# Kernel tuning notes

Hardware: AMD Instinct MI355X
Metric: run time of the kernel (lower is better)

Reference implementation:

```python
import jax, jax.numpy as jnp
import numpy as np

N_NODES = 50000
N_EDGES = 800000
K_HOPS = 4
F_IN, F_HID, A_DIM = 6, 128, 3


def gcn_norm(edge_index, edge_weight, num_nodes):
    # TAGConv(normalize=True) uses gcn_norm WITHOUT added self-loops:
    # norm = D^{-1/2}[src] * w * D^{-1/2}[dst], deg computed at target (col).
    row, col = edge_index[0], edge_index[1]
    deg = jax.ops.segment_sum(edge_weight, col, num_segments=num_nodes)
    deg_inv_sqrt = jnp.where(deg > 0, jax.lax.rsqrt(deg), 0.0)
    return deg_inv_sqrt[row] * edge_weight * deg_inv_sqrt[col]


def tag_conv(x, edge_index, norm_w, W, b):
    # out = sum_{k=0..K} (A_hat^k x) @ W[k] + b ; W: [K+1, in, out]
    row, col = edge_index[0], edge_index[1]
    out = x @ W[0]
    xk = x
    for k in range(1, W.shape[0]):
        # one sparse propagation hop: gather at src, scale, scatter-add at dst
        xk = jax.ops.segment_sum(norm_w[:, None] * xk[row], col, num_segments=x.shape[0])
        out = out + xk @ W[k]
    return out + b


def setup_inputs() -> dict:
    key = jax.random.key(0)
    ks = jax.random.split(key, 5)
    x = jax.random.normal(ks[0], (N_NODES, F_IN), dtype=jnp.float32)
    edge_index = jax.random.randint(ks[1], (2, N_EDGES), 0, N_NODES, dtype=jnp.int32)
    edge_weight = jax.random.uniform(ks[2], (N_EDGES,), dtype=jnp.float32)
    s1 = float(1.0 / np.sqrt(F_IN))
    s2 = float(1.0 / np.sqrt(F_HID))
    W1 = jax.random.uniform(ks[3], (K_HOPS + 1, F_IN, F_HID), minval=-s1, maxval=s1, dtype=jnp.float32)
    b1 = jnp.zeros((F_HID,), jnp.float32)
    W2 = jax.random.uniform(ks[4], (K_HOPS + 1, F_HID, 2 * A_DIM), minval=-s2, maxval=s2, dtype=jnp.float32)
    b2 = jnp.zeros((2 * A_DIM,), jnp.float32)
    return {"x": x, "edge_index": edge_index, "edge_weight": edge_weight,
            "W1": W1, "b1": b1, "W2": W2, "b2": b2}


def reference(x, edge_index, edge_weight, W1, b1, W2, b2):
    norm_w = gcn_norm(edge_index, edge_weight, x.shape[0])
    h = jax.nn.relu(tag_conv(x, edge_index, norm_w, W1, b1))
    out = tag_conv(h, edge_index, norm_w, W2, b2)
    mu = jnp.tanh(out[..., :A_DIM])
    logvar = jnp.tanh(out[..., A_DIM:])
    sigma = jnp.exp(2.0 * logvar)
    return mu, sigma
```

## Files before the change

kernel.cpp:

```cpp
#include <hip/hip_runtime.h>

#define NN 50000
#define NE 800000
#define KH 4
#define FIN 6
#define FH 128
#define FO 6
#define ADIM 3
#define NN6 (NN * 6)
#define NN8 (NN * 8)
#define NBKT 196
#define EPB 2048
#define NPB 391
#define CAP 6144
#define ROWMASK 0xFFFFFu
#define GFUSE 2048
#define NEPAD (NE + NBKT * 1024)

typedef unsigned int u32;
typedef _Float16 f16;
typedef f16 f16x8 __attribute__((ext_vector_type(8)));

struct __align__(8) Edge { u32 r; float w; };

__device__ __forceinline__ float h2f_bits(u32 hb) {
    union { unsigned short us; f16 h; } c; c.us = (unsigned short)hb; return (float)c.h;
}
__device__ __forceinline__ u32 f2h_bits(float f) {
    union { unsigned short us; f16 h; } c; c.h = (f16)f; return (u32)c.us;
}
__device__ __forceinline__ u32 pack2(float a, float b) {
    return f2h_bits(a) | (f2h_bits(b) << 16);
}

__global__ void bucket_hist(const int* __restrict__ col, u32* __restrict__ ghist) {
    __shared__ u32 h[NBKT];
    for (int t = threadIdx.x; t < NBKT; t += 256) h[t] = 0;
    __syncthreads();
    int base = blockIdx.x * EPB;
#pragma unroll
    for (int i = 0; i < EPB / 256; ++i) {
        int e = base + i * 256 + threadIdx.x;
        if (e < NE) atomicAdd(&h[((u32)col[e]) >> 8], 1u);
    }
    __syncthreads();
    for (int t = threadIdx.x; t < NBKT; t += 256)
        if (h[t]) atomicAdd(&ghist[t], h[t]);
}

__global__ void bucket_scan(const u32* __restrict__ ghist, u32* __restrict__ bbase,
                            u32* __restrict__ bcur) {
    __shared__ u32 sh[256];
    int t = threadIdx.x;
    u32 v = (t < NBKT) ? ghist[t] : 0;
    sh[t] = v;
    __syncthreads();
    for (int off = 1; off < 256; off <<= 1) {
        u32 u = (t >= off) ? sh[t - off] : 0;
        __syncthreads();
        sh[t] += u;
        __syncthreads();
    }
    if (t < NBKT) { bbase[t] = sh[t] - v; bcur[t] = sh[t] - v; }
    if (t == NBKT - 1) bbase[NBKT] = sh[t];
}

__global__ __launch_bounds__(256) void partition_kernel(
        const int* __restrict__ row, const int* __restrict__ col,
        const float* __restrict__ w, u32* __restrict__ bcur,
        Edge* __restrict__ etmp) {
    __shared__ u32 hcnt[NBKT];
    __shared__ u32 hloc[NBKT];
    __shared__ u32 hglb[NBKT];
    __shared__ u32 smeta[EPB];
    __shared__ float swt[EPB];
    __shared__ u32 sgid[EPB];
    __shared__ u32 sc[256];
    for (int t = threadIdx.x; t < NBKT; t += 256) hcnt[t] = 0;
    __syncthreads();
    int base = blockIdx.x * EPB;
    u32 m_[8]; float w_[8]; u32 b_[8]; u32 rk_[8]; int v_[8];
#pragma unroll
    for (int i = 0; i < 8; ++i) {
        int e = base + i * 256 + threadIdx.x;
        v_[i] = e < NE;
        if (v_[i]) {
            u32 c = (u32)col[e];
            u32 r = (u32)row[e];
            b_[i] = c >> 8;
            m_[i] = ((c & 255u) << 20) | r;
            w_[i] = w[e];
            rk_[i] = atomicAdd(&hcnt[b_[i]], 1u);
        }
    }
    __syncthreads();
    {
        int t = threadIdx.x;
        u32 v = (t < NBKT) ? hcnt[t] : 0;
        sc[t] = v;
        __syncthreads();
        for (int off = 1; off < 256; off <<= 1) {
            u32 u = (t >= off) ? sc[t - off] : 0;
            __syncthreads();
            sc[t] += u;
            __syncthreads();
        }
        if (t < NBKT) hloc[t] = sc[t] - v;
    }
    __syncthreads();
    for (int t = threadIdx.x; t < NBKT; t += 256)
        if (hcnt[t]) hglb[t] = atomicAdd(&bcur[t], hcnt[t]);
    __syncthreads();
#pragma unroll
    for (int i = 0; i < 8; ++i) if (v_[i]) {
        u32 slot = hloc[b_[i]] + rk_[i];
        smeta[slot] = m_[i];
        swt[slot] = w_[i];
        sgid[slot] = hglb[b_[i]] + rk_[i];
    }
    __syncthreads();
    int tot = NE - base; if (tot > EPB) tot = EPB;
    for (int s = threadIdx.x; s < tot; s += 256) {
        Edge ed; ed.r = smeta[s]; ed.w = swt[s];
        etmp[sgid[s]] = ed;
    }
}

__global__ __launch_bounds__(256) void bucket_csr(
        const u32* __restrict__ bbase, const Edge* __restrict__ etmp,
        u32* __restrict__ edges, int* __restrict__ offs, int* __restrict__ eoff,
        float* __restrict__ dinv) {
    int b = blockIdx.x;
    int t = threadIdx.x;
    u32 s = bbase[b], e = bbase[b + 1];
    int cnt = (int)(e - s);
    u32 rb = s + (u32)b * 1024u;
    int node0 = b << 8;
    int nloc = NN - node0; if (nloc > 256) nloc = 256;
    __shared__ u32 ncnt[256];
    __shared__ float nsum[256];
    __shared__ u32 ncur[256];
    __shared__ u32 sc[256];
    __shared__ u32 stage[CAP];
    ncnt[t] = 0; nsum[t] = 0.f;
    __syncthreads();
    for (int i = t; i < cnt; i += 256) {
        Edge ed = etmp[s + i];
        u32 cl = ed.r >> 20;
        atomicAdd(&ncnt[cl], 1u);
        atomicAdd(&nsum[cl], ed.w);
    }
    __syncthreads();
    u32 v = ncnt[t];
    u32 pv = (v + 3u) & ~3u;
    sc[t] = pv;
    __syncthreads();
    for (int off = 1; off < 256; off <<= 1) {
        u32 u = (t >= off) ? sc[t - off] : 0;
        __syncthreads();
        sc[t] += u;
        __syncthreads();
    }
    u32 excl = sc[t] - pv;
    u32 ptot = sc[255];
    ncur[t] = excl;
    if (t < nloc) {
        offs[node0 + t] = (int)(rb + excl);
        eoff[node0 + t] = (int)(rb + excl + pv);
        float d = nsum[t];
        dinv[node0 + t] = d > 0.f ? rsqrtf(d) : 0.f;
    }
    __syncthreads();
    for (int i = t; i < cnt; i += 256) {
        Edge ed = etmp[s + i];
        u32 cl = ed.r >> 20;
        u32 slot = atomicAdd(&ncur[cl], 1u);
        u32 pw = (ed.r & ROWMASK) | (f2h_bits(ed.w) << 16);
        if (slot < CAP) stage[slot] = pw;
        else edges[rb + slot] = pw;
    }
    if (t < nloc) {
        for (u32 slot = excl + v; slot < excl + pv; ++slot) {
            if (slot < CAP) stage[slot] = 0u;
            else edges[rb + slot] = 0u;
        }
    }
    __syncthreads();
    int lim = (int)(ptot < CAP ? ptot : CAP);
    for (int i = t; i < lim; i += 256) edges[rb + i] = stage[i];
}

__global__ void pad_x(const float* __restrict__ x, f16* __restrict__ xpad) {
    int t = blockIdx.x * blockDim.x + threadIdx.x;
    if (t >= NN8) return;
    int n = t >> 3, c = t & 7;
    xpad[t] = (c < 6) ? (f16)x[n * 6 + c] : (f16)0.f;
}

__device__ __forceinline__ void gath(const f16* __restrict__ xp, u32 r, float w,
                                     float& a0, float& a1, float& a2,
                                     float& a3, float& a4, float& a5) {
    f16x8 v = *(const f16x8*)(xp + (size_t)r * 8);
    a0 += w * (float)v[0]; a1 += w * (float)v[1]; a2 += w * (float)v[2];
    a3 += w * (float)v[3]; a4 += w * (float)v[4]; a5 += w * (float)v[5];
}

#define HOP_HEAD \
    int t = blockIdx.x * blockDim.x + threadIdx.x; \
    int n = t >> 2, j = t & 3; \
    if (n >= NN) return; \
    int s = offs[n], e = eoff[n]; \
    float a0 = 0.f, a1 = 0.f, a2 = 0.f, a3 = 0.f, a4 = 0.f, a5 = 0.f;

#define HOP_REDUCE \
    _Pragma("unroll") \
    for (int d = 1; d < 4; d <<= 1) { \
        a0 += __shfl_xor(a0, d); a1 += __shfl_xor(a1, d); a2 += __shfl_xor(a2, d); \
        a3 += __shfl_xor(a3, d); a4 += __shfl_xor(a4, d); a5 += __shfl_xor(a5, d); \
    }

__global__ void hop4(const int* __restrict__ offs, const int* __restrict__ eoff,
                     const u32* __restrict__ edges,
                     const f16* __restrict__ xprev, const float* __restrict__ yadd,
                     f16* __restrict__ xnext) {
    HOP_HEAD
    for (int i = s + 4 * j; i < e; i += 16) {
        int4 q = *(const int4*)(edges + i);
        { u32 wd = (u32)q.x; gath(xprev, wd & 0xFFFFu, h2f_bits(wd >> 16), a0, a1, a2, a3, a4, a5); }
        { u32 wd = (u32)q.y; gath(xprev, wd & 0xFFFFu, h2f_bits(wd >> 16), a0, a1, a2, a3, a4, a5); }
        { u32 wd = (u32)q.z; gath(xprev, wd & 0xFFFFu, h2f_bits(wd >> 16), a0, a1, a2, a3, a4, a5); }
        { u32 wd = (u32)q.w; gath(xprev, wd & 0xFFFFu, h2f_bits(wd >> 16), a0, a1, a2, a3, a4, a5); }
    }
    HOP_REDUCE
    float v0 = j == 0 ? a0 : j == 1 ? a2 : j == 2 ? a4 : 0.f;
    float v1 = j == 0 ? a1 : j == 1 ? a3 : j == 2 ? a5 : 0.f;
    if (yadd && j < 3) {
        v0 += yadd[(size_t)n * 32 + 2 * j];
        v1 += yadd[(size_t)n * 32 + 2 * j + 1];
    }
    ((u32*)xnext)[(size_t)n * 4 + j] = pack2(v0, v1);
}

__global__ void hop4_norm(const int* __restrict__ offs, const int* __restrict__ eoff,
                          u32* __restrict__ edges,
                          const float* __restrict__ dinv, const f16* __restrict__ xpad,
                          f16* __restrict__ xnext) {
    HOP_HEAD
    float dn = dinv[n];
    for (int i = s + 4 * j; i < e; i += 16) {
        int4 q = *(const int4*)(edges + i);
        int4 nq;
        {
            u32 wd = (u32)q.x; u32 r = wd & 0xFFFFu;
            float wn = h2f_bits(wd >> 16) * dn * dinv[r];
            nq.x = (int)(r | (f2h_bits(wn) << 16));
            gath(xpad, r, wn, a0, a1, a2, a3, a4, a5);
        }
        {
            u32 wd = (u32)q.y; u32 r = wd & 0xFFFFu;
            float wn = h2f_bits(wd >> 16) * dn * dinv[r];
            nq.y = (int)(r | (f2h_bits(wn) << 16));
            gath(xpad, r, wn, a0, a1, a2, a3, a4, a5);
        }
        {
            u32 wd = (u32)q.z; u32 r = wd & 0xFFFFu;
            float wn = h2f_bits(wd >> 16) * dn * dinv[r];
            nq.z = (int)(r | (f2h_bits(wn) << 16));
            gath(xpad, r, wn, a0, a1, a2, a3, a4, a5);
        }
        {
            u32 wd = (u32)q.w; u32 r = wd & 0xFFFFu;
            float wn = h2f_bits(wd >> 16) * dn * dinv[r];
            nq.w = (int)(r | (f2h_bits(wn) << 16));
            gath(xpad, r, wn, a0, a1, a2, a3, a4, a5);
        }
        *(int4*)(edges + i) = nq;
    }
    HOP_REDUCE
    float v0 = j == 0 ? a0 : j == 1 ? a2 : j == 2 ? a4 : 0.f;
    float v1 = j == 0 ? a1 : j == 1 ? a3 : j == 2 ? a5 : 0.f;
    ((u32*)xnext)[(size_t)n * 4 + j] = pack2(v0, v1);
}

__global__ void hop4_final(const int* __restrict__ offs, const int* __restrict__ eoff,
                           const u32* __restrict__ edges,
                           const f16* __restrict__ xprev, const float* __restrict__ y0,
                           float* __restrict__ out) {
    HOP_HEAD
    for (int i = s + 4 * j; i < e; i += 16) {
        int4 q = *(const int4*)(edges + i);
        { u32 wd = (u32)q.x; gath(xprev, wd & 0xFFFFu, h2f_bits(wd >> 16), a0, a1, a2, a3, a4, a5); }
        { u32 wd = (u32)q.y; gath(xprev, wd & 0xFFFFu, h2f_bits(wd >> 16), a0, a1, a2, a3, a4, a5); }
        { u32 wd = (u32)q.z; gath(xprev, wd & 0xFFFFu, h2f_bits(wd >> 16), a0, a1, a2, a3, a4, a5); }
        { u32 wd = (u32)q.w; gath(xprev, wd & 0xFFFFu, h2f_bits(wd >> 16), a0, a1, a2, a3, a4, a5); }
    }
    HOP_REDUCE
    if (j < 3) {
        float mv = (j == 0 ? a0 : j == 1 ? a1 : a2) + y0[(size_t)n * 32 + j];
        float sv = (j == 0 ? a3 : j == 1 ? a4 : a5) + y0[(size_t)n * 32 + 3 + j];
        out[n * ADIM + j] = tanhf(mv);
        out[NN * ADIM + n * ADIM + j] = expf(2.f * tanhf(sv));
    }
}

__global__ __launch_bounds__(256) void fused_dense_kernel(
        const float* __restrict__ x, const f16* __restrict__ xs,
        const float* __restrict__ W1, const float* __restrict__ b1,
        const float* __restrict__ W2, const float* __restrict__ b2,
        float* __restrict__ ys, f16* __restrict__ y4h) {
    __shared__ float sin_[2][32];
    __shared__ float sh[2][128];
    int t = threadIdx.x;
    int f = t & 127, half = t >> 7;
    float w1r[30];
#pragma unroll
    for (int i = 0; i < 30; ++i) w1r[i] = W1[i * FH + f];
    float b1r = b1[f];
    bool bact = t < 240;
    int bn = t / 120;
    int rem = t % 120;
    int ka = rem >> 2;
    int q  = rem & 3;
    int k2 = ka / 6, a2 = ka - k2 * 6;
    float w2r[32];
#pragma unroll
    for (int i = 0; i < 32; ++i)
        w2r[i] = bact ? W2[((size_t)k2 * FH + q * 32 + i) * FO + a2] : 0.f;
    float badd = (bact && k2 == 0 && q == 0) ? b2[a2] : 0.f;

    for (int n0 = blockIdx.x * 2; n0 < NN; n0 += GFUSE * 2) {
        if (t < 60) {
            int nn = t / 30, c = t - nn * 30;
            int n = n0 + nn;
            float v;
            if (c < 6) v = x[n * 6 + c];
            else       v = (float)xs[(size_t)((c - 6) / 6) * NN8 + n * 8 + (c - 6) % 6];
            sin_[nn][c] = v;
        }
        __syncthreads();
        {
            float s = b1r;
#pragma unroll
            for (int i = 0; i < 30; ++i) s += sin_[half][i] * w1r[i];
            sh[half][f] = s > 0.f ? s : 0.f;
        }
        __syncthreads();
        if (bact) {
            float s = badd;
            const float* hr = &sh[bn][q * 32];
#pragma unroll
            for (int i = 0; i < 32; ++i) s += hr[i] * w2r[i];
            s += __shfl_xor(s, 1);
            s += __shfl_xor(s, 2);
            if (q == 0) {
                if (ka < 24) ys[(size_t)(n0 + bn) * 32 + ka] = s;
                else         y4h[(size_t)(n0 + bn) * 8 + (ka - 24)] = (f16)s;
            }
        }
    }
}

extern "C" void kernel_launch(void* const* d_in, const int* in_sizes, int n_in,
                              void* d_out, int out_size, void* d_ws, size_t ws_size,
                              hipStream_t stream) {
    const float* x  = (const float*)d_in[0];
    const int*   ei = (const int*)d_in[1];
    const float* ew = (const float*)d_in[2];
    const float* W1 = (const float*)d_in[3];
    const float* b1 = (const float*)d_in[4];
    const float* W2 = (const float*)d_in[5];
    const float* b2 = (const float*)d_in[6];
    float* out = (float*)d_out;

    const int* row = ei;
    const int* col = ei + NE;

    f16*   xpad  = (f16*)d_ws;
    f16*   xs    = xpad + NN8;
    f16*   y4h   = xs + (size_t)KH * NN8;
    f16*   za    = y4h + NN8;
    f16*   zb    = za + NN8;
    float* ys    = (float*)(zb + NN8);
    Edge*  etmp  = (Edge*)(ys + (size_t)NN * 32);
    u32*   edges = (u32*)(etmp + NE);
    u32*   ghist = edges + NEPAD;
    u32*   bbase = ghist + NBKT;
    u32*   bcur  = bbase + NBKT + 1;
    int*   offs  = (int*)(bcur + NBKT);
    int*   eoff  = offs + NN;
    float* dinv  = (float*)(eoff + NN);

    const int B = 256;
    const int gHop = (NN * 4 + B - 1) / B;
    const int gPad = (NN8 + B - 1) / B;

    hipMemsetAsync(ghist, 0, NBKT * sizeof(u32), stream);
    bucket_hist<<<NPB, B, 0, stream>>>(col, ghist);
    bucket_scan<<<1, B, 0, stream>>>(ghist, bbase, bcur);
    partition_kernel<<<NPB, B, 0, stream>>>(row, col, ew, bcur, etmp);
    bucket_csr<<<NBKT, B, 0, stream>>>(bbase, etmp, edges, offs, eoff, dinv);
    pad_x<<<gPad, B, 0, stream>>>(x, xpad);

    hop4_norm<<<gHop, B, 0, stream>>>(offs, eoff, edges, dinv, xpad, xs);
    for (int k = 2; k <= KH; ++k)
        hop4<<<gHop, B, 0, stream>>>(offs, eoff, edges,
                                     xs + (size_t)(k - 2) * NN8, nullptr,
                                     xs + (size_t)(k - 1) * NN8);

    fused_dense_kernel<<<GFUSE, B, 0, stream>>>(x, xs, W1, b1, W2, b2, ys, y4h);

    hop4<<<gHop, B, 0, stream>>>(offs, eoff, edges, y4h, ys + 18, za);
    hop4<<<gHop, B, 0, stream>>>(offs, eoff, edges, za, ys + 12, zb);
    hop4<<<gHop, B, 0, stream>>>(offs, eoff, edges, zb, ys + 6, za);
    hop4_final<<<gHop, B, 0, stream>>>(offs, eoff, edges, za, ys, out);
}
```

Before: 153.4 us.

## Restructure fused dense kernel to process four nodes per block with shuffles

The fused dense layer kernel now handles four nodes per block iteration, one wavefront per node. Each lane computes two hidden features and broadcasts inputs via wave shuffles instead of staging them in shared memory. Hidden activations are stored packed as fp16 pairs and read back with vector loads. The second-layer reduction now spans two lanes instead of four, using 64 weight registers per thread. This halves the loop trip count and removes one barrier per node pair, at the cost of higher register pressure and fp16 rounding of hidden activations.

```diff
diff --git a/kernel.cpp b/kernel.cpp
--- a/kernel.cpp
+++ b/kernel.cpp
@@ -308,55 +308,71 @@
         const float* __restrict__ W1, const float* __restrict__ b1,
         const float* __restrict__ W2, const float* __restrict__ b2,
         float* __restrict__ ys, f16* __restrict__ y4h) {
-    __shared__ float sin_[2][32];
-    __shared__ float sh[2][128];
+    __shared__ u32 sh16[4][68];
     int t = threadIdx.x;
-    int f = t & 127, half = t >> 7;
-    float w1r[30];
-#pragma unroll
-    for (int i = 0; i < 30; ++i) w1r[i] = W1[i * FH + f];
-    float b1r = b1[f];
+    int lane = t & 63, wv = t >> 6;
+    float w1r0[30], w1r1[30];
+#pragma unroll
+    for (int i = 0; i < 30; ++i) {
+        w1r0[i] = W1[i * FH + 2 * lane];
+        w1r1[i] = W1[i * FH + 2 * lane + 1];
+    }
+    float b10 = b1[2 * lane], b11 = b1[2 * lane + 1];
     bool bact = t < 240;
-    int bn = t / 120;
-    int rem = t % 120;
-    int ka = rem >> 2;
-    int q  = rem & 3;
+    int bn = t / 60;
+    int rem = t % 60;
+    int ka = rem >> 1, q = rem & 1;
     int k2 = ka / 6, a2 = ka - k2 * 6;
-    float w2r[32];
-#pragma unroll
-    for (int i = 0; i < 32; ++i)
-        w2r[i] = bact ? W2[((size_t)k2 * FH + q * 32 + i) * FO + a2] : 0.f;
+    float w2r[64];
+#pragma unroll
+    for (int i = 0; i < 64; ++i)
+        w2r[i] = bact ? W2[((size_t)k2 * FH + q * 64 + i) * FO + a2] : 0.f;
     float badd = (bact && k2 == 0 && q == 0) ? b2[a2] : 0.f;
 
-    for (int n0 = blockIdx.x * 2; n0 < NN; n0 += GFUSE * 2) {
-        if (t < 60) {
-            int nn = t / 30, c = t - nn * 30;
-            int n = n0 + nn;
-            float v;
-            if (c < 6) v = x[n * 6 + c];
-            else       v = (float)xs[(size_t)((c - 6) / 6) * NN8 + n * 8 + (c - 6) % 6];
-            sin_[nn][c] = v;
-        }
-        __syncthreads();
-        {
-            float s = b1r;
-#pragma unroll
-            for (int i = 0; i < 30; ++i) s += sin_[half][i] * w1r[i];
-            sh[half][f] = s > 0.f ? s : 0.f;
-        }
+    for (int n0 = blockIdx.x * 4; n0 < NN; n0 += GFUSE * 4) {
+        int na = n0 + wv;
+        float vin = 0.f;
+        if (lane < 6) vin = x[na * 6 + lane];
+        else if (lane < 30) {
+            int l6 = lane - 6;
+            vin = (float)xs[(size_t)(l6 / 6) * NN8 + na * 8 + l6 % 6];
+        }
+        float hA = b10, hB = b11;
+#pragma unroll
+        for (int i = 0; i < 30; ++i) {
+            float xi = __shfl(vin, i);
+            hA = fmaf(xi, w1r0[i], hA);
+            hB = fmaf(xi, w1r1[i], hB);
+        }
+        hA = hA > 0.f ? hA : 0.f;
+        hB = hB > 0.f ? hB : 0.f;
+        sh16[wv][lane] = pack2(hA, hB);
         __syncthreads();
         if (bact) {
-            float s = badd;
-            const float* hr = &sh[bn][q * 32];
-#pragma unroll
-            for (int i = 0; i < 32; ++i) s += hr[i] * w2r[i];
+            float s = 0.f;
+            const u32* hw = &sh16[bn][q * 32];
+#pragma unroll
+            for (int i4 = 0; i4 < 8; ++i4) {
+                uint4 hv = *(const uint4*)(hw + 4 * i4);
+                u32 w0 = hv.x, w1 = hv.y, w2w = hv.z, w3 = hv.w;
+                s = fmaf(h2f_bits(w0 & 0xFFFFu), w2r[i4 * 8 + 0], s);
+                s = fmaf(h2f_bits(w0 >> 16),     w2r[i4 * 8 + 1], s);
+                s = fmaf(h2f_bits(w1 & 0xFFFFu), w2r[i4 * 8 + 2], s);
+                s = fmaf(h2f_bits(w1 >> 16),     w2r[i4 * 8 + 3], s);
+                s = fmaf(h2f_bits(w2w & 0xFFFFu), w2r[i4 * 8 + 4], s);
+                s = fmaf(h2f_bits(w2w >> 16),     w2r[i4 * 8 + 5], s);
+                s = fmaf(h2f_bits(w3 & 0xFFFFu), w2r[i4 * 8 + 6], s);
+                s = fmaf(h2f_bits(w3 >> 16),     w2r[i4 * 8 + 7], s);
+            }
             s += __shfl_xor(s, 1);
-            s += __shfl_xor(s, 2);
             if (q == 0) {
-                if (ka < 24) ys[(size_t)(n0 + bn) * 32 + ka] = s;
-                else         y4h[(size_t)(n0 + bn) * 8 + (ka - 24)] = (f16)s;
+                float v = s + badd;
+                int n = n0 + bn;
+                if (ka < 24) ys[(size_t)n * 32 + ka] = v;
+                else         y4h[(size_t)n * 8 + (ka - 24)] = (f16)v;
             }
         }
+        __syncthreads();
     }
 }
 
```

Measured after the change: 178.9 us. +16.6%, slower.

## Rewrite fused dense kernel as one node per thread with transposed weights

Applied to the files above, without the earlier changes.

The fused dense layer moves from a block-cooperative scheme (two nodes per block iteration, shared memory and two barriers per step) to one thread per node. Each thread keeps its 30 inputs and 30 outputs in registers and loops over the 128 hidden units. The weights are transposed once inside the scan kernel so every thread reads the same contiguous row, which should become uniform/scalar loads. This removes the per-node barriers and shuffle reductions, at the cost of heavy register pressure and only about 196 blocks of parallelism.

```diff
diff --git a/kernel.cpp b/kernel.cpp
--- a/kernel.cpp
+++ b/kernel.cpp
@@ -14,7 +14,6 @@
 #define NPB 391
 #define CAP 6144
 #define ROWMASK 0xFFFFFu
-#define GFUSE 2048
 #define NEPAD (NE + NBKT * 1024)
 
 typedef unsigned int u32;
@@ -49,7 +48,9 @@
 }
 
 __global__ void bucket_scan(const u32* __restrict__ ghist, u32* __restrict__ bbase,
-                            u32* __restrict__ bcur) {
+                            u32* __restrict__ bcur,
+                            const float* __restrict__ W1, const float* __restrict__ W2,
+                            float* __restrict__ W1T, float* __restrict__ W2T) {
     __shared__ u32 sh[256];
     int t = threadIdx.x;
     u32 v = (t < NBKT) ? ghist[t] : 0;
@@ -63,6 +64,12 @@
     }
     if (t < NBKT) { bbase[t] = sh[t] - v; bcur[t] = sh[t] - v; }
     if (t == NBKT - 1) bbase[NBKT] = sh[t];
+    for (int idx = t; idx < 30 * FH; idx += 256) {
+        int f = idx / 30, i = idx - f * 30;
+        W1T[idx] = W1[i * FH + f];
+        int k = i / 6, a = i - k * 6;
+        W2T[idx] = W2[((size_t)k * FH + f) * FO + a];
+    }
 }
 
 __global__ __launch_bounds__(256) void partition_kernel(
@@ -305,59 +312,49 @@
 
 __global__ __launch_bounds__(256) void fused_dense_kernel(
         const float* __restrict__ x, const f16* __restrict__ xs,
-        const float* __restrict__ W1, const float* __restrict__ b1,
-        const float* __restrict__ W2, const float* __restrict__ b2,
+        const float* __restrict__ W1T, const float* __restrict__ b1,
+        const float* __restrict__ W2T, const float* __restrict__ b2,
         float* __restrict__ ys, f16* __restrict__ y4h) {
-    __shared__ float sin_[2][32];
-    __shared__ float sh[2][128];
-    int t = threadIdx.x;
-    int f = t & 127, half = t >> 7;
-    float w1r[30];
-#pragma unroll
-    for (int i = 0; i < 30; ++i) w1r[i] = W1[i * FH + f];
-    float b1r = b1[f];
-    bool bact = t < 240;
-    int bn = t / 120;
-    int rem = t % 120;
-    int ka = rem >> 2;
-    int q  = rem & 3;
-    int k2 = ka / 6, a2 = ka - k2 * 6;
-    float w2r[32];
-#pragma unroll
-    for (int i = 0; i < 32; ++i)
-        w2r[i] = bact ? W2[((size_t)k2 * FH + q * 32 + i) * FO + a2] : 0.f;
-    float badd = (bact && k2 == 0 && q == 0) ? b2[a2] : 0.f;
-
-    for (int n0 = blockIdx.x * 2; n0 < NN; n0 += GFUSE * 2) {
-        if (t < 60) {
-            int nn = t / 30, c = t - nn * 30;
-            int n = n0 + nn;
-            float v;
-            if (c < 6) v = x[n * 6 + c];
-            else       v = (float)xs[(size_t)((c - 6) / 6) * NN8 + n * 8 + (c - 6) % 6];
-            sin_[nn][c] = v;
-        }
-        __syncthreads();
-        {
-            float s = b1r;
-#pragma unroll
-            for (int i = 0; i < 30; ++i) s += sin_[half][i] * w1r[i];
-            sh[half][f] = s > 0.f ? s : 0.f;
-        }
-        __syncthreads();
-        if (bact) {
-            float s = badd;
-            const float* hr = &sh[bn][q * 32];
-#pragma unroll
-            for (int i = 0; i < 32; ++i) s += hr[i] * w2r[i];
-            s += __shfl_xor(s, 1);
-            s += __shfl_xor(s, 2);
-            if (q == 0) {
-                if (ka < 24) ys[(size_t)(n0 + bn) * 32 + ka] = s;
-                else         y4h[(size_t)(n0 + bn) * 8 + (ka - 24)] = (f16)s;
-            }
-        }
-    }
+    int n = blockIdx.x * 256 + threadIdx.x;
+    if (n >= NN) return;
+    float in[30];
+    {
+        const float* xr = x + (size_t)n * 6;
+        float2 v0 = *(const float2*)xr;
+        float2 v1 = *(const float2*)(xr + 2);
+        float2 v2 = *(const float2*)(xr + 4);
+        in[0] = v0.x; in[1] = v0.y; in[2] = v1.x;
+        in[3] = v1.y; in[4] = v2.x; in[5] = v2.y;
+    }
+#pragma unroll
+    for (int k = 0; k < 4; ++k) {
+        f16x8 v = *(const f16x8*)(xs + (size_t)k * NN8 + (size_t)n * 8);
+#pragma unroll
+        for (int c = 0; c < 6; ++c) in[6 + k * 6 + c] = (float)v[c];
+    }
+    float acc[30];
+#pragma unroll
+    for (int o = 0; o < 30; ++o) acc[o] = (o < 6) ? b2[o] : 0.f;
+#pragma unroll 2
+    for (int f = 0; f < FH; ++f) {
+        const float* w1c = W1T + f * 30;
+        float h = b1[f];
+#pragma unroll
+        for (int i = 0; i < 30; ++i) h = fmaf(in[i], w1c[i], h);
+        h = h > 0.f ? h : 0.f;
+        const float* w2c = W2T + f * 30;
+#pragma unroll
+        for (int o = 0; o < 30; ++o) acc[o] = fmaf(h, w2c[o], acc[o]);
+    }
+    float* yr = ys + (size_t)n * 32;
+#pragma unroll
+    for (int o4 = 0; o4 < 6; ++o4)
+        *(float4*)(yr + o4 * 4) = make_float4(acc[o4 * 4], acc[o4 * 4 + 1],
+                                              acc[o4 * 4 + 2], acc[o4 * 4 + 3]);
+    u32* yh = (u32*)(y4h + (size_t)n * 8);
+    yh[0] = pack2(acc[24], acc[25]);
+    yh[1] = pack2(acc[26], acc[27]);
+    yh[2] = pack2(acc[28], acc[29]);
 }
 
 extern "C" void kernel_launch(void* const* d_in, const int* in_sizes, int n_in,
@@ -381,7 +378,9 @@
     f16*   za    = y4h + NN8;
     f16*   zb    = za + NN8;
     float* ys    = (float*)(zb + NN8);
-    Edge*  etmp  = (Edge*)(ys + (size_t)NN * 32);
+    float* W1T   = ys + (size_t)NN * 32;
+    float* W2T   = W1T + 30 * FH;
+    Edge*  etmp  = (Edge*)(W2T + 30 * FH);
     u32*   edges = (u32*)(etmp + NE);
     u32*   ghist = edges + NEPAD;
     u32*   bbase = ghist + NBKT;
@@ -393,10 +392,11 @@
     const int B = 256;
     const int gHop = (NN * 4 + B - 1) / B;
     const int gPad = (NN8 + B - 1) / B;
+    const int gFD  = (NN + B - 1) / B;
 
     hipMemsetAsync(ghist, 0, NBKT * sizeof(u32), stream);
     bucket_hist<<<NPB, B, 0, stream>>>(col, ghist);
-    bucket_scan<<<1, B, 0, stream>>>(ghist, bbase, bcur);
+    bucket_scan<<<1, B, 0, stream>>>(ghist, bbase, bcur, W1, W2, W1T, W2T);
     partition_kernel<<<NPB, B, 0, stream>>>(row, col, ew, bcur, etmp);
     bucket_csr<<<NBKT, B, 0, stream>>>(bbase, etmp, edges, offs, eoff, dinv);
     pad_x<<<gPad, B, 0, stream>>>(x, xpad);
@@ -407,7 +407,7 @@
                                      xs + (size_t)(k - 2) * NN8, nullptr,
                                      xs + (size_t)(k - 1) * NN8);
 
-    fused_dense_kernel<<<GFUSE, B, 0, stream>>>(x, xs, W1, b1, W2, b2, ys, y4h);
+    fused_dense_kernel<<<gFD, B, 0, stream>>>(x, xs, W1T, b1, W2T, b2, ys, y4h);
 
     hop4<<<gHop, B, 0, stream>>>(offs, eoff, edges, y4h, ys + 18, za);
     hop4<<<gHop, B, 0, stream>>>(offs, eoff, edges, za, ys + 12, zb);
```

Result: slower. 163.8 us (+6.8%).
